# Optimization experiments

Hardware: AMD Instinct MI355X
Metric: run time of the kernel (lower is better)

Reference implementation:

```python
import jax, jax.numpy as jnp
import numpy as np

NUM_GRAPHS = 32
NODES_PER_GRAPH = 256
N = NUM_GRAPHS * NODES_PER_GRAPH
IN_CH, HID, OUT_CH = 64, 256, 32
K = 20
SPACE, PROP = 3, 2
NEG_SLOPE = 0.01  # F.leaky_relu default
BIG = 1e9         # cross-graph distance mask


def _glorot(key, shape):
    fan_in, fan_out = shape
    lim = (6.0 / (fan_in + fan_out)) ** 0.5
    return jax.random.uniform(key, shape, jnp.float32, -lim, lim)


def setup_inputs() -> dict:
    key = jax.random.key(0)
    ks = jax.random.split(key, 16)
    inp = {
        "x": jax.random.normal(ks[0], (N, IN_CH), jnp.float32),
        "batch": jnp.repeat(jnp.arange(NUM_GRAPHS, dtype=jnp.int32), NODES_PER_GRAPH),
    }
    dims = [(IN_CH, HID), (HID, HID), (HID, OUT_CH)]
    i = 1
    for li, (cin, cout) in enumerate(dims, start=1):
        inp[f"Ws{li}"] = _glorot(ks[i], (cin, SPACE)); i += 1
        inp[f"bs{li}"] = jnp.zeros((SPACE,), jnp.float32)
        inp[f"Wh{li}"] = _glorot(ks[i], (cin, PROP)); i += 1
        inp[f"bh{li}"] = jnp.zeros((PROP,), jnp.float32)
        inp[f"Wo{li}"] = _glorot(ks[i], (cin + PROP, cout)); i += 1
        inp[f"bo{li}"] = jnp.zeros((cout,), jnp.float32)
    return inp


def gravnet_conv(x, mask_add, Ws, bs, Wh, bh, Wo, bo):
    s = x @ Ws + bs                                     # [N,3] learned coords
    h = x @ Wh + bh                                     # [N,2] propagate feats
    s2 = jnp.sum(s * s, axis=1)
    d2 = s2[:, None] + s2[None, :] - 2.0 * (s @ s.T)    # [N,N] squared dists
    d2 = jnp.maximum(d2, 0.0) + mask_add                # block within-graph only
    neg_d2, idx = jax.lax.top_k(-d2, K)                 # kNN (includes self)
    w = jnp.exp(10.0 * neg_d2)                          # exp(-10 * d^2)
    agg = jnp.einsum('nk,nkp->np', w, h[idx])           # aggr='add'
    return jnp.concatenate([agg, x], axis=-1) @ Wo + bo  # lin(cat([out, x]))


def _leaky(h):
    return jnp.where(h >= 0, h, NEG_SLOPE * h)


def reference(x, batch,
              Ws1, bs1, Wh1, bh1, Wo1, bo1,
              Ws2, bs2, Wh2, bh2, Wo2, bo2,
              Ws3, bs3, Wh3, bh3, Wo3, bo3):
    mask_add = jnp.where(batch[:, None] == batch[None, :], 0.0, BIG).astype(x.dtype)
    # dropout p=0.0 -> identity
    h = _leaky(gravnet_conv(x, mask_add, Ws1, bs1, Wh1, bh1, Wo1, bo1))
    h = _leaky(gravnet_conv(h, mask_add, Ws2, bs2, Wh2, bh2, Wo2, bo2))
    out = gravnet_conv(h, mask_add, Ws3, bs3, Wh3, bh3, Wo3, bo3)
    # get_zero_nodes: first node of each contiguous graph segment
    b = jnp.concatenate([jnp.zeros((1,), batch.dtype), batch])
    diff = (b[1:] - b[:-1]).at[0].set(1)
    first_idx = jnp.nonzero(diff != 0, size=NUM_GRAPHS)[0]
    return out[first_idx]
```

## Files before the change

### kernel.cpp

```cpp
#include <hip/hip_runtime.h>
#include <hip/hip_bf16.h>


#define NGRAPH 32
#define GN 256
#define NTOT (NGRAPH*GN)
#define KNN 20
#define CTS 129

typedef __attribute__((ext_vector_type(8))) short bf16x8;
typedef __attribute__((ext_vector_type(4))) float f32x4;

__device__ __forceinline__ ushort f2bf(float x) {
    union { float f; unsigned u; } a; a.f = x;
    unsigned r = a.u + 0x7FFFu + ((a.u >> 16) & 1u);
    return (ushort)(r >> 16);
}
__device__ __forceinline__ float bf2f(ushort h) {
    union { unsigned u; float f; } b; b.u = ((unsigned)h) << 16;
    return b.f;
}
__device__ __forceinline__ bf16x8 ld8(const ushort* p) {
    return *reinterpret_cast<const bf16x8*>(p);
}
__device__ __forceinline__ unsigned pack2(ushort a, ushort b) {
    return (unsigned)a | ((unsigned)b << 16);
}

#define DPP_MIN(v, ctrl, rmask) { \
    unsigned _t = (unsigned)__builtin_amdgcn_update_dpp((int)(v), (int)(v), ctrl, rmask, 0xf, false); \
    (v) = _t < (v) ? _t : (v); }
__device__ __forceinline__ unsigned wave_min_u32(unsigned v) {
    DPP_MIN(v, 0x111, 0xf)
    DPP_MIN(v, 0x112, 0xf)
    DPP_MIN(v, 0x114, 0xf)
    DPP_MIN(v, 0x118, 0xf)
    DPP_MIN(v, 0x142, 0xa)
    DPP_MIN(v, 0x143, 0xc)
    return (unsigned)__builtin_amdgcn_readlane((int)v, 63);
}
#define DPP_ADD(v, ctrl, rmask) { \
    float _t = __int_as_float(__builtin_amdgcn_update_dpp(0, __float_as_int(v), ctrl, rmask, 0xf, true)); \
    (v) += _t; }
__device__ __forceinline__ float wave_sum_f32(float v) {
    DPP_ADD(v, 0x111, 0xf)
    DPP_ADD(v, 0x112, 0xf)
    DPP_ADD(v, 0x114, 0xf)
    DPP_ADD(v, 0x118, 0xf)
    DPP_ADD(v, 0x142, 0xa)
    DPP_ADD(v, 0x143, 0xc)
    return __int_as_float(__builtin_amdgcn_readlane(__float_as_int(v), 63));
}

__device__ __forceinline__ void knn_extract(
    unsigned ua, unsigned ub, unsigned uc, unsigned ud,
    float2 hA, float2 hB, float2 hC, float2 hD,
    int lane, float& out0, float& out1)
{
    float acc0 = 0.f, acc1 = 0.f;
#pragma unroll 1
    for (int it = 0; it < KNN; ++it) {
        unsigned m1 = ua < ub ? ua : ub;
        unsigned m2 = uc < ud ? uc : ud;
        unsigned bv = m1 < m2 ? m1 : m2;
        unsigned gv = wave_min_u32(bv);
        float d2 = __uint_as_float(gv);
        if (d2 > 2.0f) break;
        float w = __expf(-10.0f * d2);
        unsigned long long mask = __ballot(bv == gv);
        int wl = __ffsll(mask) - 1;
        if (lane == wl) {
            float h0, h1;
            if (ua == gv)      { h0 = hA.x; h1 = hA.y; ua = 0xFFFFFFFFu; }
            else if (ub == gv) { h0 = hB.x; h1 = hB.y; ub = 0xFFFFFFFFu; }
            else if (uc == gv) { h0 = hC.x; h1 = hC.y; uc = 0xFFFFFFFFu; }
            else               { h0 = hD.x; h1 = hD.y; ud = 0xFFFFFFFFu; }
            acc0 = fmaf(w, h0, acc0);
            acc1 = fmaf(w, h1, acc1);
        }
    }
    out0 = wave_sum_f32(acc0);
    out1 = wave_sum_f32(acc1);
}

__global__ __launch_bounds__(256) void knn1_mega(
    const float* __restrict__ X,
    const float* __restrict__ Ws1, const float* __restrict__ bs1,
    const float* __restrict__ Wh1, const float* __restrict__ bh1,
    const float* __restrict__ Wo1, const float* __restrict__ Wo2,
    const float* __restrict__ bs2, const float* __restrict__ bh2,
    const float* __restrict__ bs3, const float* __restrict__ bh3,
    ushort* __restrict__ Wt1hi, ushort* __restrict__ Wt1lo,
    ushort* __restrict__ Wt2hi, ushort* __restrict__ Wt2lo,
    ushort* __restrict__ Xhi, ushort* __restrict__ Xlo,
    float* __restrict__ s2, float* __restrict__ h2p,
    float* __restrict__ s3, float* __restrict__ h3p,
    float* __restrict__ agg)
{
    __shared__ float sh5[256 * 5];
    int b = blockIdx.x, tid = threadIdx.x;
    if (b < 512) {
        int g = b >> 4;
        const float* Xg = X + (size_t)g * (GN * 64);
        {
            float a0 = 0.f, a1 = 0.f, a2 = 0.f, a3 = 0.f, a4 = 0.f;
            const float* xr = Xg + tid * 64;
#pragma unroll 4
            for (int c0 = 0; c0 < 64; c0 += 4) {
                float4 v = *reinterpret_cast<const float4*>(&xr[c0]);
                float xv[4] = {v.x, v.y, v.z, v.w};
#pragma unroll
                for (int j = 0; j < 4; ++j) {
                    int c = c0 + j;
                    a0 = fmaf(xv[j], Ws1[c * 3 + 0], a0);
                    a1 = fmaf(xv[j], Ws1[c * 3 + 1], a1);
                    a2 = fmaf(xv[j], Ws1[c * 3 + 2], a2);
                    a3 = fmaf(xv[j], Wh1[c * 2 + 0], a3);
                    a4 = fmaf(xv[j], Wh1[c * 2 + 1], a4);
                }
            }
            sh5[tid * 5 + 0] = a0 + bs1[0];
            sh5[tid * 5 + 1] = a1 + bs1[1];
            sh5[tid * 5 + 2] = a2 + bs1[2];
            sh5[tid * 5 + 3] = a3 + bh1[0];
            sh5[tid * 5 + 4] = a4 + bh1[1];
        }
        __syncthreads();
        int lane = tid & 63, wid = tid >> 6;
        float sjx[4], sjy[4], sjz[4], s2j[4];
        float2 hs[4];
#pragma unroll
        for (int t = 0; t < 4; ++t) {
            int j = lane + 64 * t;
            float x = sh5[j * 5 + 0], y = sh5[j * 5 + 1], z = sh5[j * 5 + 2];
            sjx[t] = x; sjy[t] = y; sjz[t] = z;
            s2j[t] = x * x + y * y + z * z;
            hs[t] = make_float2(sh5[j * 5 + 3], sh5[j * 5 + 4]);
        }
        int rbase = (b & 15) * 16 + wid * 4;
#pragma unroll 1
        for (int rr = 0; rr < 4; ++rr) {
            int rl = rbase + rr;
            float s0 = sh5[rl * 5 + 0], s1v = sh5[rl * 5 + 1], s2v = sh5[rl * 5 + 2];
            float s2row = s0 * s0 + s1v * s1v + s2v * s2v;
            unsigned key[4];
#pragma unroll
            for (int t = 0; t < 4; ++t) {
                float dot = s0 * sjx[t] + s1v * sjy[t] + s2v * sjz[t];
                float d2 = s2row + s2j[t] - 2.0f * dot;
                key[t] = __float_as_uint(d2 > 0.f ? d2 : 0.f);
            }
            float a0, a1;
            knn_extract(key[0], key[1], key[2], key[3], hs[0], hs[1], hs[2], hs[3], lane, a0, a1);
            if (lane == 0) {
                agg[(g * GN + rl) * 2 + 0] = a0;
                agg[(g * GN + rl) * 2 + 1] = a1;
            }
        }
    } else if (b < 832) {
        int t = (b - 512) * 256 + tid;
        if (t < 65536) {
            int n = t >> 8, c = t & 255;
            float v = Wo2[(size_t)(2 + c) * 256 + n];
            ushort hi = f2bf(v);
            Wt2hi[n * 256 + c] = hi;
            Wt2lo[n * 256 + c] = f2bf(v - bf2f(hi));
        } else {
            int u = t - 65536;
            int n = u >> 6, c = u & 63;
            float v = Wo1[(size_t)(2 + c) * 256 + n];
            ushort hi = f2bf(v);
            Wt1hi[n * 64 + c] = hi;
            Wt1lo[n * 64 + c] = f2bf(v - bf2f(hi));
        }
    } else if (b < 1152) {
        int u = (b - 832) * 256 + tid;
        if (u < 24576)      s2[u] = bs2[u % 3];
        else if (u < 40960) { int w = u - 24576; h2p[w] = bh2[w & 1]; }
        else if (u < 65536) { int w = u - 40960; s3[w] = bs3[w % 3]; }
        else                { int w = u - 65536; h3p[w] = bh3[w & 1]; }
    } else {
        int t = (b - 1152) * 256 + tid;
        float2 v = *reinterpret_cast<const float2*>(&X[(size_t)t * 2]);
        ushort hx = f2bf(v.x), hy = f2bf(v.y);
        Xhi[t * 2 + 0] = hx; Xlo[t * 2 + 0] = f2bf(v.x - bf2f(hx));
        Xhi[t * 2 + 1] = hy; Xlo[t * 2 + 1] = f2bf(v.y - bf2f(hy));
    }
}

__global__ __launch_bounds__(256) void knn_kernel(
    const float* __restrict__ s, const float* __restrict__ h,
    float* __restrict__ agg)
{
    int gw = (int)(blockIdx.x * 4 + (threadIdx.x >> 6));
    int lane = threadIdx.x & 63;
    int base = gw & ~(GN - 1);
    float s0 = s[gw * 3 + 0], s1v = s[gw * 3 + 1], s2v = s[gw * 3 + 2];
    float s2row = s0 * s0 + s1v * s1v + s2v * s2v;
    unsigned key[4]; float2 hs[4];
#pragma unroll
    for (int t = 0; t < 4; ++t) {
        int j = base + lane + 64 * t;
        float x = s[j * 3 + 0], y = s[j * 3 + 1], z = s[j * 3 + 2];
        float dot = s0 * x + s1v * y + s2v * z;
        float d2 = s2row + (x * x + y * y + z * z) - 2.0f * dot;
        key[t] = __float_as_uint(d2 > 0.f ? d2 : 0.f);
        hs[t] = *reinterpret_cast<const float2*>(&h[(size_t)j * 2]);
    }
    float a0, a1;
    knn_extract(key[0], key[1], key[2], key[3], hs[0], hs[1], hs[2], hs[3], lane, a0, a1);
    if (lane == 0) {
        agg[gw * 2 + 0] = a0;
        agg[gw * 2 + 1] = a1;
    }
}

template<int K, int CMODE>
__global__ __launch_bounds__(512) void gemm_fused(
    const ushort* __restrict__ Ahi, const ushort* __restrict__ Alo,
    const ushort* __restrict__ Bhi, const ushort* __restrict__ Blo,
    const float* __restrict__ Wfull, const float* __restrict__ bias,
    const float* __restrict__ agg,
    float* __restrict__ Cf, ushort* __restrict__ Chi, ushort* __restrict__ Clo,
    const float* __restrict__ Wsn, const float* __restrict__ Whn,
    float* __restrict__ s_out, float* __restrict__ h_out)
{
    __shared__ float CT[64 * CTS];
    __shared__ float part[64 * 8 * 5];

    const int tid = threadIdx.x;
    const int lane = tid & 63, wid = tid >> 6;
    const int wm = wid >> 2, wn = wid & 3;
    const int m0 = blockIdx.x * 64, n0 = blockIdx.y * 128;

    f32x4 acc[2][2];
#pragma unroll
    for (int mi = 0; mi < 2; ++mi)
#pragma unroll
        for (int ni = 0; ni < 2; ++ni)
            acc[mi][ni] = (f32x4){0.f, 0.f, 0.f, 0.f};

#pragma unroll 2
    for (int kof = 0; kof < K; kof += 32) {
        int kch = kof + (lane >> 4) * 8;
        bf16x8 ah[2], al[2], bh[2], bl[2];
#pragma unroll
        for (int mi = 0; mi < 2; ++mi) {
            size_t off = (size_t)(m0 + wm * 32 + mi * 16 + (lane & 15)) * K + kch;
            ah[mi] = ld8(Ahi + off); al[mi] = ld8(Alo + off);
        }
#pragma unroll
        for (int ni = 0; ni < 2; ++ni) {
            size_t off = (size_t)(n0 + wn * 32 + ni * 16 + (lane & 15)) * K + kch;
            bh[ni] = ld8(Bhi + off); bl[ni] = ld8(Blo + off);
        }
#pragma unroll
        for (int mi = 0; mi < 2; ++mi)
#pragma unroll
            for (int ni = 0; ni < 2; ++ni) {
                acc[mi][ni] = __builtin_amdgcn_mfma_f32_16x16x32_bf16(ah[mi], bh[ni], acc[mi][ni], 0, 0, 0);
                acc[mi][ni] = __builtin_amdgcn_mfma_f32_16x16x32_bf16(ah[mi], bl[ni], acc[mi][ni], 0, 0, 0);
                acc[mi][ni] = __builtin_amdgcn_mfma_f32_16x16x32_bf16(al[mi], bh[ni], acc[mi][ni], 0, 0, 0);
            }
    }

#pragma unroll
    for (int ni = 0; ni < 2; ++ni) {
        int nl = wn * 32 + ni * 16 + (lane & 15);
        int n = n0 + nl;
        float w0 = Wfull[n], w1 = Wfull[256 + n], bz = bias[n];
#pragma unroll
        for (int mi = 0; mi < 2; ++mi) {
            int mb = wm * 32 + mi * 16 + ((lane >> 4) << 2);
#pragma unroll
            for (int r = 0; r < 4; ++r) {
                int ml = mb + r, m = m0 + ml;
                float v = acc[mi][ni][r] + fmaf(agg[m * 2 + 0], w0, fmaf(agg[m * 2 + 1], w1, bz));
                v = v >= 0.f ? v : 0.01f * v;
                CT[ml * CTS + nl] = v;
                if (CMODE == 1 && (m & 255) == 0) Cf[(m >> 8) * 256 + n] = v;
            }
        }
    }
    __syncthreads();

    if (CMODE == 0) {
        int row = tid >> 3, cbase = (tid & 7) * 16;
        size_t m = (size_t)(m0 + row);
#pragma unroll
        for (int j = 0; j < 2; ++j) {
            int c = cbase + j * 8;
            ushort hi[8], lo[8];
#pragma unroll
            for (int t = 0; t < 8; ++t) {
                float v = CT[row * CTS + c + t];
                hi[t] = f2bf(v);
                lo[t] = f2bf(v - bf2f(hi[t]));
            }
            uint4 wh = make_uint4(pack2(hi[0], hi[1]), pack2(hi[2], hi[3]),
                                  pack2(hi[4], hi[5]), pack2(hi[6], hi[7]));
            uint4 wl = make_uint4(pack2(lo[0], lo[1]), pack2(lo[2], lo[3]),
                                  pack2(lo[4], lo[5]), pack2(lo[6], lo[7]));
            *reinterpret_cast<uint4*>(&Chi[m * 256 + n0 + c]) = wh;
            *reinterpret_cast<uint4*>(&Clo[m * 256 + n0 + c]) = wl;
        }
    }

    {
        int row = tid & 63, sub = tid >> 6;
        float p0 = 0.f, p1 = 0.f, p2 = 0.f, p3 = 0.f, p4 = 0.f;
#pragma unroll
        for (int i = 0; i < 16; ++i) {
            int c = sub * 16 + i;
            float v = CT[row * CTS + c];
            int n = n0 + c;
            p0 = fmaf(v, Wsn[n * 3 + 0], p0);
            p1 = fmaf(v, Wsn[n * 3 + 1], p1);
            p2 = fmaf(v, Wsn[n * 3 + 2], p2);
            p3 = fmaf(v, Whn[n * 2 + 0], p3);
            p4 = fmaf(v, Whn[n * 2 + 1], p4);
        }
        float* pp = &part[(row * 8 + sub) * 5];
        pp[0] = p0; pp[1] = p1; pp[2] = p2; pp[3] = p3; pp[4] = p4;
    }
    __syncthreads();
    if (tid < 320) {
        int row = tid / 5, o = tid - row * 5;
        float sum = 0.f;
#pragma unroll
        for (int k = 0; k < 8; ++k) sum += part[(row * 8 + k) * 5 + o];
        if (o < 3) atomicAdd(&s_out[(m0 + row) * 3 + o], sum);
        else       atomicAdd(&h_out[(m0 + row) * 2 + (o - 3)], sum);
    }
}

__global__ __launch_bounds__(256) void knn3_final(
    const float* __restrict__ s, const float* __restrict__ h,
    const float* __restrict__ h2c,
    const float* __restrict__ Wo, const float* __restrict__ bo,
    float* __restrict__ out)
{
    __shared__ float aggL[2];
    __shared__ float pm[8][32];
    int g = blockIdx.x, tid = threadIdx.x;
    if (tid < 64) {
        int lane = tid;
        int base = g * GN, row = g * GN;
        float s0 = s[row * 3 + 0], s1v = s[row * 3 + 1], s2v = s[row * 3 + 2];
        float s2row = s0 * s0 + s1v * s1v + s2v * s2v;
        unsigned key[4]; float2 hs[4];
#pragma unroll
        for (int t = 0; t < 4; ++t) {
            int j = base + lane + 64 * t;
            float x = s[j * 3 + 0], y = s[j * 3 + 1], z = s[j * 3 + 2];
            float dot = s0 * x + s1v * y + s2v * z;
            float d2 = s2row + (x * x + y * y + z * z) - 2.0f * dot;
            key[t] = __float_as_uint(d2 > 0.f ? d2 : 0.f);
            hs[t] = *reinterpret_cast<const float2*>(&h[(size_t)j * 2]);
        }
        float a0, a1;
        knn_extract(key[0], key[1], key[2], key[3], hs[0], hs[1], hs[2], hs[3], lane, a0, a1);
        if (lane == 0) { aggL[0] = a0; aggL[1] = a1; }
    }
    __syncthreads();
    int o = tid & 31, seg = tid >> 5;
    const float* xr = h2c + g * 256;
    float p = 0.f;
#pragma unroll
    for (int i = 0; i < 32; ++i) {
        int c = seg * 32 + i;
        p = fmaf(xr[c], Wo[(2 + c) * 32 + o], p);
    }
    pm[seg][o] = p;
    __syncthreads();
    if (tid < 32) {
        float acc = fmaf(aggL[0], Wo[o], fmaf(aggL[1], Wo[32 + o], bo[o]));
#pragma unroll
        for (int k = 0; k < 8; ++k) acc += pm[k][o];
        out[g * 32 + o] = acc;
    }
}

extern "C" void kernel_launch(void* const* d_in, const int* in_sizes, int n_in,
                              void* d_out, int out_size, void* d_ws, size_t ws_size,
                              hipStream_t stream) {
    const float* X   = (const float*)d_in[0];
    const float* Ws1 = (const float*)d_in[2];  const float* bs1 = (const float*)d_in[3];
    const float* Wh1 = (const float*)d_in[4];  const float* bh1 = (const float*)d_in[5];
    const float* Wo1 = (const float*)d_in[6];  const float* bo1 = (const float*)d_in[7];
    const float* Ws2 = (const float*)d_in[8];  const float* bs2 = (const float*)d_in[9];
    const float* Wh2 = (const float*)d_in[10]; const float* bh2 = (const float*)d_in[11];
    const float* Wo2 = (const float*)d_in[12]; const float* bo2 = (const float*)d_in[13];
    const float* Ws3 = (const float*)d_in[14]; const float* bs3 = (const float*)d_in[15];
    const float* Wh3 = (const float*)d_in[16]; const float* bh3 = (const float*)d_in[17];
    const float* Wo3 = (const float*)d_in[18]; const float* bo3 = (const float*)d_in[19];

    float* p = (float*)d_ws;
    float* s2   = p; p += NTOT * 3;
    float* hp2  = p; p += NTOT * 2;
    float* s3   = p; p += NTOT * 3;
    float* hp3  = p; p += NTOT * 2;
    float* aggb = p; p += NTOT * 2;
    float* h2c  = p; p += 32 * 256;
    ushort* q = (ushort*)p;
    ushort* Xhi  = q; q += (size_t)NTOT * 64;
    ushort* Xlo  = q; q += (size_t)NTOT * 64;
    ushort* h1hi = q; q += (size_t)NTOT * 256;
    ushort* h1lo = q; q += (size_t)NTOT * 256;
    ushort* Wt1hi = q; q += 256 * 64;
    ushort* Wt1lo = q; q += 256 * 64;
    ushort* Wt2hi = q; q += 256 * 256;
    ushort* Wt2lo = q; q += 256 * 256;

    knn1_mega<<<2176, 256, 0, stream>>>(X, Ws1, bs1, Wh1, bh1, Wo1, Wo2,
                                        bs2, bh2, bs3, bh3,
                                        Wt1hi, Wt1lo, Wt2hi, Wt2lo, Xhi, Xlo,
                                        s2, hp2, s3, hp3, aggb);
    gemm_fused<64, 0><<<dim3(128, 2), 512, 0, stream>>>(Xhi, Xlo, Wt1hi, Wt1lo,
                                                        Wo1, bo1, aggb,
                                                        nullptr, h1hi, h1lo,
                                                        Ws2, Wh2, s2, hp2);
    knn_kernel<<<2048, 256, 0, stream>>>(s2, hp2, aggb);
    gemm_fused<256, 1><<<dim3(128, 2), 512, 0, stream>>>(h1hi, h1lo, Wt2hi, Wt2lo,
                                                         Wo2, bo2, aggb,
                                                         h2c, nullptr, nullptr,
                                                         Ws3, Wh3, s3, hp3);
    knn3_final<<<NGRAPH, 256, 0, stream>>>(s3, hp3, h2c, Wo3, bo3, (float*)d_out);
}
```

Measured before the change: 78.77 us.

## Interleave four kNN row extractions per wave and stage graph coords in LDS

Adds a knn_rows4 helper in which each wave processes four query rows at once, interleaving their DPP min-reductions and sum-reductions so the dependency chains overlap. The layer-2 kNN kernel now loads each graph's coordinates and features into shared memory once per block, with 512 blocks each handling 16 rows instead of 2048 blocks each reading global memory per row. The early exit for distances above 2.0 is removed, and results are read from lane 63, the lane that holds the complete DPP reduction. The cost is higher register pressure from four rows of keys per lane and fewer waves in flight for layer 2.

```diff
diff --git a/kernel.cpp b/kernel.cpp
--- a/kernel.cpp
+++ b/kernel.cpp
@@ -30,6 +30,9 @@
 #define DPP_MIN(v, ctrl, rmask) { \
     unsigned _t = (unsigned)__builtin_amdgcn_update_dpp((int)(v), (int)(v), ctrl, rmask, 0xf, false); \
     (v) = _t < (v) ? _t : (v); }
+#define DPP_ADD(v, ctrl, rmask) { \
+    float _t = __int_as_float(__builtin_amdgcn_update_dpp(0, __float_as_int(v), ctrl, rmask, 0xf, true)); \
+    (v) += _t; }
 __device__ __forceinline__ unsigned wave_min_u32(unsigned v) {
     DPP_MIN(v, 0x111, 0xf)
     DPP_MIN(v, 0x112, 0xf)
@@ -39,9 +42,6 @@
     DPP_MIN(v, 0x143, 0xc)
     return (unsigned)__builtin_amdgcn_readlane((int)v, 63);
 }
-#define DPP_ADD(v, ctrl, rmask) { \
-    float _t = __int_as_float(__builtin_amdgcn_update_dpp(0, __float_as_int(v), ctrl, rmask, 0xf, true)); \
-    (v) += _t; }
 __device__ __forceinline__ float wave_sum_f32(float v) {
     DPP_ADD(v, 0x111, 0xf)
     DPP_ADD(v, 0x112, 0xf)
@@ -65,7 +65,6 @@
         unsigned bv = m1 < m2 ? m1 : m2;
         unsigned gv = wave_min_u32(bv);
         float d2 = __uint_as_float(gv);
-        if (d2 > 2.0f) break;
         float w = __expf(-10.0f * d2);
         unsigned long long mask = __ballot(bv == gv);
         int wl = __ffsll(mask) - 1;
@@ -81,6 +80,84 @@
     }
     out0 = wave_sum_f32(acc0);
     out1 = wave_sum_f32(acc1);
+}
+
+__device__ __forceinline__ void knn_rows4(
+    const float* sh5, int rbase, int lane, int growbase, float* __restrict__ agg)
+{
+    float sjx[4], sjy[4], sjz[4], s2j[4];
+    float2 hs[4];
+#pragma unroll
+    for (int t = 0; t < 4; ++t) {
+        int j = lane + 64 * t;
+        float x = sh5[j * 5 + 0], y = sh5[j * 5 + 1], z = sh5[j * 5 + 2];
+        sjx[t] = x; sjy[t] = y; sjz[t] = z;
+        s2j[t] = x * x + y * y + z * z;
+        hs[t] = make_float2(sh5[j * 5 + 3], sh5[j * 5 + 4]);
+    }
+    unsigned key[4][4];
+    float acc0[4], acc1[4];
+#pragma unroll
+    for (int r = 0; r < 4; ++r) {
+        int rl = rbase + r;
+        float s0 = sh5[rl * 5 + 0], s1v = sh5[rl * 5 + 1], s2v = sh5[rl * 5 + 2];
+        float s2row = s0 * s0 + s1v * s1v + s2v * s2v;
+#pragma unroll
+        for (int t = 0; t < 4; ++t) {
+            float dot = s0 * sjx[t] + s1v * sjy[t] + s2v * sjz[t];
+            float d2 = s2row + s2j[t] - 2.0f * dot;
+            key[r][t] = __float_as_uint(d2 > 0.f ? d2 : 0.f);
+        }
+        acc0[r] = 0.f; acc1[r] = 0.f;
+    }
+#pragma unroll 1
+    for (int it = 0; it < KNN; ++it) {
+        unsigned bv[4], gv[4];
+#pragma unroll
+        for (int r = 0; r < 4; ++r) {
+            unsigned m1 = key[r][0] < key[r][1] ? key[r][0] : key[r][1];
+            unsigned m2 = key[r][2] < key[r][3] ? key[r][2] : key[r][3];
+            bv[r] = m1 < m2 ? m1 : m2;
+            gv[r] = bv[r];
+        }
+#define KSTAGE(ctrl, rmask) { \
+        DPP_MIN(gv[0], ctrl, rmask) DPP_MIN(gv[1], ctrl, rmask) \
+        DPP_MIN(gv[2], ctrl, rmask) DPP_MIN(gv[3], ctrl, rmask) }
+        KSTAGE(0x111, 0xf) KSTAGE(0x112, 0xf) KSTAGE(0x114, 0xf)
+        KSTAGE(0x118, 0xf) KSTAGE(0x142, 0xa) KSTAGE(0x143, 0xc)
+#undef KSTAGE
+#pragma unroll
+        for (int r = 0; r < 4; ++r) {
+            unsigned g = (unsigned)__builtin_amdgcn_readlane((int)gv[r], 63);
+            float w = __expf(-10.0f * __uint_as_float(g));
+            unsigned long long mask = __ballot(bv[r] == g);
+            int wl = __ffsll(mask) - 1;
+            if (lane == wl) {
+                float h0, h1;
+                if (key[r][0] == g)      { h0 = hs[0].x; h1 = hs[0].y; key[r][0] = 0xFFFFFFFFu; }
+                else if (key[r][1] == g) { h0 = hs[1].x; h1 = hs[1].y; key[r][1] = 0xFFFFFFFFu; }
+                else if (key[r][2] == g) { h0 = hs[2].x; h1 = hs[2].y; key[r][2] = 0xFFFFFFFFu; }
+                else                     { h0 = hs[3].x; h1 = hs[3].y; key[r][3] = 0xFFFFFFFFu; }
+                acc0[r] = fmaf(w, h0, acc0[r]);
+                acc1[r] = fmaf(w, h1, acc1[r]);
+            }
+        }
+    }
+#define SSTAGE(ctrl, rmask) { \
+    DPP_ADD(acc0[0], ctrl, rmask) DPP_ADD(acc1[0], ctrl, rmask) \
+    DPP_ADD(acc0[1], ctrl, rmask) DPP_ADD(acc1[1], ctrl, rmask) \
+    DPP_ADD(acc0[2], ctrl, rmask) DPP_ADD(acc1[2], ctrl, rmask) \
+    DPP_ADD(acc0[3], ctrl, rmask) DPP_ADD(acc1[3], ctrl, rmask) }
+    SSTAGE(0x111, 0xf) SSTAGE(0x112, 0xf) SSTAGE(0x114, 0xf)
+    SSTAGE(0x118, 0xf) SSTAGE(0x142, 0xa) SSTAGE(0x143, 0xc)
+#undef SSTAGE
+    if (lane == 63) {
+#pragma unroll
+        for (int r = 0; r < 4; ++r) {
+            agg[(growbase + rbase + r) * 2 + 0] = acc0[r];
+            agg[(growbase + rbase + r) * 2 + 1] = acc1[r];
+        }
+    }
 }
 
 __global__ __launch_bounds__(256) void knn1_mega(
@@ -126,37 +203,7 @@
             sh5[tid * 5 + 4] = a4 + bh1[1];
         }
         __syncthreads();
-        int lane = tid & 63, wid = tid >> 6;
-        float sjx[4], sjy[4], sjz[4], s2j[4];
-        float2 hs[4];
-#pragma unroll
-        for (int t = 0; t < 4; ++t) {
-            int j = lane + 64 * t;
-            float x = sh5[j * 5 + 0], y = sh5[j * 5 + 1], z = sh5[j * 5 + 2];
-            sjx[t] = x; sjy[t] = y; sjz[t] = z;
-            s2j[t] = x * x + y * y + z * z;
-            hs[t] = make_float2(sh5[j * 5 + 3], sh5[j * 5 + 4]);
-        }
-        int rbase = (b & 15) * 16 + wid * 4;
-#pragma unroll 1
-        for (int rr = 0; rr < 4; ++rr) {
-            int rl = rbase + rr;
-            float s0 = sh5[rl * 5 + 0], s1v = sh5[rl * 5 + 1], s2v = sh5[rl * 5 + 2];
-            float s2row = s0 * s0 + s1v * s1v + s2v * s2v;
-            unsigned key[4];
-#pragma unroll
-            for (int t = 0; t < 4; ++t) {
-                float dot = s0 * sjx[t] + s1v * sjy[t] + s2v * sjz[t];
-                float d2 = s2row + s2j[t] - 2.0f * dot;
-                key[t] = __float_as_uint(d2 > 0.f ? d2 : 0.f);
-            }
-            float a0, a1;
-            knn_extract(key[0], key[1], key[2], key[3], hs[0], hs[1], hs[2], hs[3], lane, a0, a1);
-            if (lane == 0) {
-                agg[(g * GN + rl) * 2 + 0] = a0;
-                agg[(g * GN + rl) * 2 + 1] = a1;
-            }
-        }
+        knn_rows4(sh5, (b & 15) * 16 + (tid >> 6) * 4, tid & 63, g * GN, agg);
     } else if (b < 832) {
         int t = (b - 512) * 256 + tid;
         if (t < 65536) {
@@ -188,31 +235,21 @@
     }
 }
 
-__global__ __launch_bounds__(256) void knn_kernel(
+__global__ __launch_bounds__(256) void knn2_kernel(
     const float* __restrict__ s, const float* __restrict__ h,
     float* __restrict__ agg)
 {
-    int gw = (int)(blockIdx.x * 4 + (threadIdx.x >> 6));
-    int lane = threadIdx.x & 63;
-    int base = gw & ~(GN - 1);
-    float s0 = s[gw * 3 + 0], s1v = s[gw * 3 + 1], s2v = s[gw * 3 + 2];
-    float s2row = s0 * s0 + s1v * s1v + s2v * s2v;
-    unsigned key[4]; float2 hs[4];
-#pragma unroll
-    for (int t = 0; t < 4; ++t) {
-        int j = base + lane + 64 * t;
-        float x = s[j * 3 + 0], y = s[j * 3 + 1], z = s[j * 3 + 2];
-        float dot = s0 * x + s1v * y + s2v * z;
-        float d2 = s2row + (x * x + y * y + z * z) - 2.0f * dot;
-        key[t] = __float_as_uint(d2 > 0.f ? d2 : 0.f);
-        hs[t] = *reinterpret_cast<const float2*>(&h[(size_t)j * 2]);
-    }
-    float a0, a1;
-    knn_extract(key[0], key[1], key[2], key[3], hs[0], hs[1], hs[2], hs[3], lane, a0, a1);
-    if (lane == 0) {
-        agg[gw * 2 + 0] = a0;
-        agg[gw * 2 + 1] = a1;
-    }
+    __shared__ float sh5[256 * 5];
+    int b = blockIdx.x, tid = threadIdx.x;
+    int g = b & 31, chunk = b >> 5;
+    int node = g * GN + tid;
+    sh5[tid * 5 + 0] = s[node * 3 + 0];
+    sh5[tid * 5 + 1] = s[node * 3 + 1];
+    sh5[tid * 5 + 2] = s[node * 3 + 2];
+    sh5[tid * 5 + 3] = h[node * 2 + 0];
+    sh5[tid * 5 + 4] = h[node * 2 + 1];
+    __syncthreads();
+    knn_rows4(sh5, chunk * 16 + (tid >> 6) * 4, tid & 63, g * GN, agg);
 }
 
 template<int K, int CMODE>
@@ -360,7 +397,7 @@
         }
         float a0, a1;
         knn_extract(key[0], key[1], key[2], key[3], hs[0], hs[1], hs[2], hs[3], lane, a0, a1);
-        if (lane == 0) { aggL[0] = a0; aggL[1] = a1; }
+        if (lane == 63) { aggL[0] = a0; aggL[1] = a1; }
     }
     __syncthreads();
     int o = tid & 31, seg = tid >> 5;
@@ -420,7 +457,7 @@
                                                         Wo1, bo1, aggb,
                                                         nullptr, h1hi, h1lo,
                                                         Ws2, Wh2, s2, hp2);
-    knn_kernel<<<2048, 256, 0, stream>>>(s2, hp2, aggb);
+    knn2_kernel<<<512, 256, 0, stream>>>(s2, hp2, aggb);
     gemm_fused<256, 1><<<dim3(128, 2), 512, 0, stream>>>(h1hi, h1lo, Wt2hi, Wt2lo,
                                                          Wo2, bo2, aggb,
                                                          h2c, nullptr, nullptr,
```

New measurement: 77.13 us. 1.02x faster.
